# Performance work log

Hardware: AMD Instinct MI355X
Metric: run time of the kernel (lower is better)

The kernel has to match this reference:

```python
import jax, jax.numpy as jnp
import numpy as np

B, T, F = 16, 512, 512
H, D = 8, 64  # heads, key_dim (latent_dim)
EPS = 1e-3    # keras LayerNormalization default epsilon


def layer_norm(x, g, b):
    mu = jnp.mean(x, axis=-1, keepdims=True)
    var = jnp.mean(jnp.square(x - mu), axis=-1, keepdims=True)
    return (x - mu) * jax.lax.rsqrt(var + EPS) * g + b


def setup_inputs() -> dict:
    key = jax.random.key(0)
    ks = jax.random.split(key, 16)
    s = 0.02
    return {
        "x": jax.random.normal(ks[0], (B, T, F), jnp.float32),
        # MultiHeadAttention params (keras layout)
        "Wq": jax.random.normal(ks[1], (F, H, D), jnp.float32) * s,
        "bq": jnp.zeros((H, D), jnp.float32),
        "Wk": jax.random.normal(ks[2], (F, H, D), jnp.float32) * s,
        "bk": jnp.zeros((H, D), jnp.float32),
        "Wv": jax.random.normal(ks[3], (F, H, D), jnp.float32) * s,
        "bv": jnp.zeros((H, D), jnp.float32),
        "Wo": jax.random.normal(ks[4], (H, D, F), jnp.float32) * s,
        "bo": jnp.zeros((F,), jnp.float32),
        "ln1_g": jnp.ones((F,), jnp.float32),
        "ln1_b": jnp.zeros((F,), jnp.float32),
        # GRU (reset_after=True, recurrent_activation=sigmoid, activation=relu)
        "gru_k": jax.random.normal(ks[5], (F, 3 * F), jnp.float32) * s,
        "gru_rk": jax.random.normal(ks[6], (F, 3 * F), jnp.float32) * s,
        "gru_b": jnp.zeros((2, 3 * F), jnp.float32),  # [input_bias, recurrent_bias]
        # Dense
        "Wd": jax.random.normal(ks[7], (F, F), jnp.float32) * s,
        "bd": jnp.zeros((F,), jnp.float32),
        "ln2_g": jnp.ones((F,), jnp.float32),
        "ln2_b": jnp.zeros((F,), jnp.float32),
    }


def mha(x, Wq, bq, Wk, bk, Wv, bv, Wo, bo):
    q = jnp.einsum("btf,fhd->bthd", x, Wq) + bq
    k = jnp.einsum("bsf,fhd->bshd", x, Wk) + bk
    v = jnp.einsum("bsf,fhd->bshd", x, Wv) + bv
    scores = jnp.einsum("bthd,bshd->bhts", q, k) / jnp.sqrt(jnp.float32(D))
    attn = jax.nn.softmax(scores, axis=-1)
    ctx = jnp.einsum("bhts,bshd->bthd", attn, v)
    return jnp.einsum("bthd,hdf->btf", ctx, Wo) + bo


def gru(x, gru_k, gru_rk, gru_b):
    # keras GRU, reset_after=True: precompute input projections once
    xp = x @ gru_k + gru_b[0]            # [B,T,3F]
    rb = gru_b[1]                        # recurrent bias [3F]
    xp_t = jnp.transpose(xp, (1, 0, 2))  # time-major [T,B,3F]

    def step(h, xt):
        rec = h @ gru_rk + rb
        xz, xr, xh = jnp.split(xt, 3, axis=-1)
        rz, rr, rh = jnp.split(rec, 3, axis=-1)
        z = jax.nn.sigmoid(xz + rz)
        r = jax.nn.sigmoid(xr + rr)
        hh = jax.nn.relu(xh + r * rh)    # activation='relu'
        h_new = z * h + (1.0 - z) * hh
        return h_new, h_new

    h0 = jnp.zeros((x.shape[0], gru_rk.shape[0]), x.dtype)
    _, ys = jax.lax.scan(step, h0, xp_t)
    return jnp.transpose(ys, (1, 0, 2))  # [B,T,F]


def reference(x, Wq, bq, Wk, bk, Wv, bv, Wo, bo, ln1_g, ln1_b,
              gru_k, gru_rk, gru_b, Wd, bd, ln2_g, ln2_b):
    a = mha(x, Wq, bq, Wk, bk, Wv, bv, Wo, bo)
    x1 = layer_norm(a + x, ln1_g, ln1_b)
    g = gru(x1, gru_k, gru_rk, gru_b)
    d = g @ Wd + bd
    return layer_norm(d + x1, ln2_g, ln2_b)
```

## Files before the change

kernel.cpp:

```cpp
#include <hip/hip_runtime.h>
#include <math.h>

#define GRID_WGS 128

typedef __attribute__((ext_vector_type(8))) short bf16x8;
typedef __attribute__((ext_vector_type(4))) float f32x4;
typedef __attribute__((ext_vector_type(4))) unsigned short us4;

static __device__ __forceinline__ float sigmoidf_(float x) {
    return 1.0f / (1.0f + __expf(-x));
}
static __device__ __forceinline__ unsigned short f2bf(float f) {
    unsigned int u = __float_as_uint(f);
    u += 0x7fffu + ((u >> 16) & 1u);
    return (unsigned short)(u >> 16);
}
static __device__ __forceinline__ float bfbits2f(unsigned int b) {
    return __uint_as_float(b << 16);
}
static __device__ __forceinline__ void gload_lds16(const void* g, void* l) {
    __builtin_amdgcn_global_load_lds(
        (const __attribute__((address_space(1))) unsigned int*)g,
        (__attribute__((address_space(3))) unsigned int*)l, 16, 0, 0);
}

__global__ __launch_bounds__(256)
void prep(const float* __restrict__ x, unsigned short* __restrict__ xb,
          const float* __restrict__ bq, const float* __restrict__ bk,
          const float* __restrict__ bv, float* __restrict__ bqkv,
          const float* __restrict__ Wq, const float* __restrict__ Wk,
          const float* __restrict__ Wv, const float* __restrict__ Wo,
          const float* __restrict__ gruk, const float* __restrict__ Wd,
          unsigned short* __restrict__ wqkvT, unsigned short* __restrict__ woT,
          unsigned short* __restrict__ gkT, unsigned short* __restrict__ wdT,
          unsigned int* __restrict__ hbufz, unsigned int* __restrict__ Z)
{
    __shared__ float tile[32][33];
    const int bid = blockIdx.x, tid = threadIdx.x;
    if (bid < 4096) {
        const int i = (bid * 256 + tid) * 4;
        const float4 v = *(const float4*)(x + i);
        const us4 o = {f2bf(v.x), f2bf(v.y), f2bf(v.z), f2bf(v.w)};
        *(us4*)(xb + i) = o;
    } else if (bid < 4102) {
        const int i = (bid - 4096) * 256 + tid;
        bqkv[i] = (i < 512) ? bq[i] : ((i < 1024) ? bk[i - 512] : bv[i - 1024]);
    } else if (bid < 6150) {
        int t = bid - 4102;
        const float* in; unsigned short* out; int N;
        if      (t < 256)  { in = Wq;   out = wqkvT;               N = 512;  }
        else if (t < 512)  { in = Wk;   out = wqkvT + 256 * 1024;  N = 512;  t -= 256;  }
        else if (t < 768)  { in = Wv;   out = wqkvT + 512 * 1024;  N = 512;  t -= 512;  }
        else if (t < 1024) { in = Wo;   out = woT;                 N = 512;  t -= 768;  }
        else if (t < 1792) { in = gruk; out = gkT;                 N = 1536; t -= 1024; }
        else               { in = Wd;   out = wdT;                 N = 512;  t -= 1792; }
        const int tilesx = N / 32;
        const int n0 = (t % tilesx) * 32, k0 = (t / tilesx) * 32;
        const int c = tid & 31, r8 = tid >> 5;
#pragma unroll
        for (int i = 0; i < 4; ++i) {
            const int k = r8 + i * 8;
            tile[k][c] = in[(size_t)(k0 + k) * N + n0 + c];
        }
        __syncthreads();
#pragma unroll
        for (int i = 0; i < 4; ++i) {
            const int n = r8 + i * 8;
            out[(size_t)(n0 + n) * 512 + k0 + c] = f2bf(tile[c][n]);
        }
    } else if (bid == 6150) {
        for (int i = tid; i < 8192; i += 256) hbufz[i] = 0u;
    } else {
        for (int i = tid; i < 2048; i += 256) Z[i] = 0u;
    }
}

__global__ __launch_bounds__(256)
void gemm_bf16(const unsigned short* __restrict__ A, const unsigned short* __restrict__ Bt,
               const float* __restrict__ bias, const float* __restrict__ resid,
               float* __restrict__ C, unsigned short* __restrict__ Cb,
               int M, int N, int K)
{
    __shared__ unsigned short As[128 * 64];
    __shared__ unsigned short Bs[128 * 64];
    const int tid = threadIdx.x;
    const int wave = tid >> 6, lane = tid & 63;
    const int bm = blockIdx.x * 128, bn = blockIdx.y * 128;
    const int wr = wave >> 1, wc = wave & 1;
    const int stR = lane >> 3;
    const int stC = (lane & 7) * 8;

    const unsigned short* Abase = A + (size_t)(bm + wave * 32 + stR) * K + stC;
    const unsigned short* Bbase = Bt + (size_t)(bn + wave * 32 + stR) * K + stC;
    unsigned short* AsW = As + wave * 2048;
    unsigned short* BsW = Bs + wave * 2048;

    f32x4 acc[4][4] = {};
    const int fr = lane & 15;
    const int fko = (lane >> 4) * 8;

    for (int k0 = 0; k0 < K; k0 += 64) {
#pragma unroll
        for (int i = 0; i < 4; ++i) {
            gload_lds16(Abase + (size_t)i * 8 * K + k0, AsW + i * 512);
            gload_lds16(Bbase + (size_t)i * 8 * K + k0, BsW + i * 512);
        }
        __syncthreads();
        bf16x8 af[4][2], bfr[4][2];
#pragma unroll
        for (int m = 0; m < 4; ++m) {
            const unsigned short* ap = As + (wr * 64 + m * 16 + fr) * 64 + fko;
            af[m][0] = *(const bf16x8*)(ap);
            af[m][1] = *(const bf16x8*)(ap + 32);
        }
#pragma unroll
        for (int n = 0; n < 4; ++n) {
            const unsigned short* bp = Bs + (wc * 64 + n * 16 + fr) * 64 + fko;
            bfr[n][0] = *(const bf16x8*)(bp);
            bfr[n][1] = *(const bf16x8*)(bp + 32);
        }
#pragma unroll
        for (int m = 0; m < 4; ++m)
#pragma unroll
            for (int n = 0; n < 4; ++n) {
                acc[m][n] = __builtin_amdgcn_mfma_f32_16x16x32_bf16(af[m][0], bfr[n][0], acc[m][n], 0, 0, 0);
                acc[m][n] = __builtin_amdgcn_mfma_f32_16x16x32_bf16(af[m][1], bfr[n][1], acc[m][n], 0, 0, 0);
            }
        __syncthreads();
    }
    const int fq = lane >> 4;
#pragma unroll
    for (int n = 0; n < 4; ++n) {
        const int col = bn + wc * 64 + n * 16 + fr;
        const float bv = bias ? bias[col] : 0.f;
#pragma unroll
        for (int m = 0; m < 4; ++m) {
#pragma unroll
            for (int j = 0; j < 4; ++j) {
                const int row = bm + wr * 64 + m * 16 + fq * 4 + j;
                float v = acc[m][n][j] + bv;
                if (resid) v += resid[(size_t)row * N + col];
                if (C)  C[(size_t)row * N + col] = v;
                if (Cb) Cb[(size_t)row * N + col] = f2bf(v);
            }
        }
    }
}

__global__ __launch_bounds__(256)
void attn_bf16(const unsigned short* __restrict__ qkv, unsigned short* __restrict__ ctxb)
{
    __shared__ unsigned short S[32][512];
    __shared__ float KV[64][69];
    const int tid = threadIdx.x;
    const int wg = blockIdx.x;
    const int qt = wg & 15, h = (wg >> 4) & 7, b = wg >> 7;
    const int r = tid >> 3, oct = tid & 7;
    const int t0 = qt * 32;
    const int ss = tid >> 2, d4 = (tid & 3) * 16;

    float4 qreg[16];
    {
        const unsigned short* qrow = qkv + ((size_t)(b * 512 + t0 + r) * 1536) + h * 64;
#pragma unroll
        for (int i = 0; i < 8; ++i) {
            const bf16x8 v = *(const bf16x8*)(qrow + i * 8);
            qreg[2 * i] = {bfbits2f((unsigned short)v[0]) * 0.125f,
                           bfbits2f((unsigned short)v[1]) * 0.125f,
                           bfbits2f((unsigned short)v[2]) * 0.125f,
                           bfbits2f((unsigned short)v[3]) * 0.125f};
            qreg[2 * i + 1] = {bfbits2f((unsigned short)v[4]) * 0.125f,
                               bfbits2f((unsigned short)v[5]) * 0.125f,
                               bfbits2f((unsigned short)v[6]) * 0.125f,
                               bfbits2f((unsigned short)v[7]) * 0.125f};
        }
    }
    for (int st = 0; st < 8; ++st) {
        {
            const unsigned short* krow =
                qkv + ((size_t)(b * 512 + st * 64 + ss) * 1536) + 512 + h * 64 + d4;
            const bf16x8 v0 = *(const bf16x8*)(krow);
            const bf16x8 v1 = *(const bf16x8*)(krow + 8);
#pragma unroll
            for (int e = 0; e < 8; ++e) {
                KV[ss][d4 + e] = bfbits2f((unsigned short)v0[e]);
                KV[ss][d4 + 8 + e] = bfbits2f((unsigned short)v1[e]);
            }
        }
        __syncthreads();
        float accd[8] = {};
#pragma unroll 4
        for (int kk = 0; kk < 16; ++kk) {
            const float4 qv = qreg[kk];
#pragma unroll
            for (int i = 0; i < 8; ++i) {
                const float4 kv = *(const float4*)&KV[oct * 8 + i][kk * 4];
                accd[i] += qv.x * kv.x + qv.y * kv.y + qv.z * kv.z + qv.w * kv.w;
            }
        }
#pragma unroll
        for (int i = 0; i < 8; ++i)
            S[r][st * 64 + oct * 8 + i] = f2bf(accd[i]);
        __syncthreads();
    }
    const int c0 = oct * 64;
    float mx = -1e30f;
#pragma unroll
    for (int c8 = 0; c8 < 8; ++c8) {
        const bf16x8 sv = *(const bf16x8*)&S[r][c0 + c8 * 8];
#pragma unroll
        for (int e = 0; e < 8; ++e) mx = fmaxf(mx, bfbits2f((unsigned short)sv[e]));
    }
    mx = fmaxf(mx, __shfl_xor(mx, 1));
    mx = fmaxf(mx, __shfl_xor(mx, 2));
    mx = fmaxf(mx, __shfl_xor(mx, 4));
    float sum = 0.f;
#pragma unroll
    for (int c8 = 0; c8 < 8; ++c8) {
        const bf16x8 sv = *(const bf16x8*)&S[r][c0 + c8 * 8];
        us4 o1, o2;
#pragma unroll
        for (int e = 0; e < 8; ++e) {
            const float p = __expf(bfbits2f((unsigned short)sv[e]) - mx);
            sum += p;
            if (e < 4) o1[e] = f2bf(p); else o2[e - 4] = f2bf(p);
        }
        *(us4*)&S[r][c0 + c8 * 8] = o1;
        *(us4*)&S[r][c0 + c8 * 8 + 4] = o2;
    }
    sum += __shfl_xor(sum, 1);
    sum += __shfl_xor(sum, 2);
    sum += __shfl_xor(sum, 4);
    const float inv = 1.0f / sum;
    __syncthreads();
    float o[8] = {};
    for (int st = 0; st < 8; ++st) {
        {
            const unsigned short* vrow =
                qkv + ((size_t)(b * 512 + st * 64 + ss) * 1536) + 1024 + h * 64 + d4;
            const bf16x8 v0 = *(const bf16x8*)(vrow);
            const bf16x8 v1 = *(const bf16x8*)(vrow + 8);
#pragma unroll
            for (int e = 0; e < 8; ++e) {
                KV[ss][d4 + e] = bfbits2f((unsigned short)v0[e]);
                KV[ss][d4 + 8 + e] = bfbits2f((unsigned short)v1[e]);
            }
        }
        __syncthreads();
#pragma unroll 2
        for (int s8 = 0; s8 < 8; ++s8) {
            const bf16x8 pv = *(const bf16x8*)&S[r][st * 64 + s8 * 8];
#pragma unroll
            for (int e = 0; e < 8; ++e) {
                const float p = bfbits2f((unsigned short)pv[e]);
                const float4 k0 = *(const float4*)&KV[s8 * 8 + e][oct * 8];
                const float4 k1 = *(const float4*)&KV[s8 * 8 + e][oct * 8 + 4];
                o[0] = fmaf(p, k0.x, o[0]); o[1] = fmaf(p, k0.y, o[1]);
                o[2] = fmaf(p, k0.z, o[2]); o[3] = fmaf(p, k0.w, o[3]);
                o[4] = fmaf(p, k1.x, o[4]); o[5] = fmaf(p, k1.y, o[5]);
                o[6] = fmaf(p, k1.z, o[6]); o[7] = fmaf(p, k1.w, o[7]);
            }
        }
        __syncthreads();
    }
    unsigned short* crow = ctxb + ((size_t)(b * 512 + t0 + r) * 512) + h * 64 + oct * 8;
    const us4 t1 = {f2bf(o[0] * inv), f2bf(o[1] * inv), f2bf(o[2] * inv), f2bf(o[3] * inv)};
    const us4 t2 = {f2bf(o[4] * inv), f2bf(o[5] * inv), f2bf(o[6] * inv), f2bf(o[7] * inv)};
    *(us4*)(crow) = t1;
    *(us4*)(crow + 4) = t2;
}

__global__ __launch_bounds__(256)
void ln_f32(const float* __restrict__ in, float* __restrict__ out,
            const float* __restrict__ g, const float* __restrict__ bb,
            unsigned short* __restrict__ outb)
{
    const int lane = threadIdx.x & 63;
    const int row = blockIdx.x * 4 + (threadIdx.x >> 6);
    const float* x = in + (size_t)row * 512;
    const float4 a = *(const float4*)(x + lane * 4);
    const float4 c = *(const float4*)(x + 256 + lane * 4);
    float s = a.x + a.y + a.z + a.w + c.x + c.y + c.z + c.w;
#pragma unroll
    for (int off = 1; off < 64; off <<= 1) s += __shfl_xor(s, off);
    const float mu = s * (1.0f / 512.0f);
    float vs = 0.f;
    vs += (a.x - mu) * (a.x - mu) + (a.y - mu) * (a.y - mu);
    vs += (a.z - mu) * (a.z - mu) + (a.w - mu) * (a.w - mu);
    vs += (c.x - mu) * (c.x - mu) + (c.y - mu) * (c.y - mu);
    vs += (c.z - mu) * (c.z - mu) + (c.w - mu) * (c.w - mu);
#pragma unroll
    for (int off = 1; off < 64; off <<= 1) vs += __shfl_xor(vs, off);
    const float rstd = rsqrtf(vs * (1.0f / 512.0f) + 1e-3f);
    const float4 g1 = *(const float4*)(g + lane * 4);
    const float4 g2 = *(const float4*)(g + 256 + lane * 4);
    const float4 b1 = *(const float4*)(bb + lane * 4);
    const float4 b2 = *(const float4*)(bb + 256 + lane * 4);
    float* y = out + (size_t)row * 512;
    const float4 o1 = {(a.x - mu) * rstd * g1.x + b1.x, (a.y - mu) * rstd * g1.y + b1.y,
                       (a.z - mu) * rstd * g1.z + b1.z, (a.w - mu) * rstd * g1.w + b1.w};
    const float4 o2 = {(c.x - mu) * rstd * g2.x + b2.x, (c.y - mu) * rstd * g2.y + b2.y,
                       (c.z - mu) * rstd * g2.z + b2.z, (c.w - mu) * rstd * g2.w + b2.w};
    *(float4*)(y + lane * 4) = o1;
    *(float4*)(y + 256 + lane * 4) = o2;
    if (outb) {
        unsigned short* yb = outb + (size_t)row * 512;
        const us4 p1 = {f2bf(o1.x), f2bf(o1.y), f2bf(o1.z), f2bf(o1.w)};
        const us4 p2 = {f2bf(o2.x), f2bf(o2.y), f2bf(o2.z), f2bf(o2.w)};
        *(us4*)(yb + lane * 4) = p1;
        *(us4*)(yb + 256 + lane * 4) = p2;
    }
}

__global__ __launch_bounds__(256, 1)
void gru_persist(const float* __restrict__ rk,
                 const unsigned short* __restrict__ xpb,
                 const float* __restrict__ rb,
                 unsigned short* __restrict__ hbuf,
                 unsigned short* __restrict__ goutb,
                 unsigned int* __restrict__ bar,
                 unsigned int* __restrict__ ctl)
{
    __shared__ int sh_part, sh_memb;
    const int tid = threadIdx.x;

    if (tid == 0) {
        unsigned int xcc;
        asm("s_getreg_b32 %0, hwreg(HW_REG_XCC_ID)" : "=s"(xcc));
        xcc &= 7u;
        const unsigned int rank =
            __hip_atomic_fetch_add(&ctl[xcc], 1u, __ATOMIC_RELAXED, __HIP_MEMORY_SCOPE_AGENT);
        __hip_atomic_fetch_add(&ctl[8], 1u, __ATOMIC_ACQ_REL, __HIP_MEMORY_SCOPE_AGENT);
        unsigned int spins = 0;
        while (__hip_atomic_load(&ctl[8], __ATOMIC_ACQUIRE, __HIP_MEMORY_SCOPE_AGENT)
               < (unsigned)GRID_WGS) {
            __builtin_amdgcn_s_sleep(1);
            if (++spins > (1u << 20)) break;
        }
        unsigned int cnt[8];
#pragma unroll
        for (int i = 0; i < 8; ++i)
            cnt[i] = __hip_atomic_load(&ctl[i], __ATOMIC_ACQUIRE, __HIP_MEMORY_SCOPE_AGENT);
        int best = 0;
#pragma unroll
        for (int i = 1; i < 8; ++i)
            if (cnt[i] > cnt[best]) best = i;
        sh_part = (xcc == (unsigned)best && rank < 8u) ? 1 : 0;
        sh_memb = (int)rank;
    }
    __syncthreads();
    if (!sh_part) return;
    const int member = sh_memb;

    const int wv = tid >> 6, l = tid & 63;
    const int wgi = member * 4 + wv;
    const int lo16 = l & 15;
    const int hi4 = l >> 4;
    const int gc = wgi * 16 + lo16;

    bf16x8 B[3][16];
#pragma unroll
    for (int g = 0; g < 3; ++g)
#pragma unroll
        for (int kt = 0; kt < 16; ++kt) {
            bf16x8 bv;
#pragma unroll
            for (int j = 0; j < 8; ++j) {
                const int k = kt * 32 + hi4 * 8 + j;
                bv[j] = (short)f2bf(rk[(size_t)k * 1536 + g * 512 + gc]);
            }
            B[g][kt] = bv;
        }
    const float rbz = rb[gc], rbr = rb[512 + gc], rbh = rb[1024 + gc];
    float hst[4] = {0.f, 0.f, 0.f, 0.f};

    float xz[4], xr[4], xh[4];
#pragma unroll
    for (int j = 0; j < 4; ++j) {
        const unsigned short* xrow = xpb + ((size_t)((hi4 * 4 + j) * 512)) * 1536 + gc;
        xz[j] = bfbits2f(xrow[0]); xr[j] = bfbits2f(xrow[512]); xh[j] = bfbits2f(xrow[1024]);
    }
    unsigned int hnb[4] = {0u, 0u, 0u, 0u};

    const unsigned short* ab0 = hbuf + lo16 * 512 + hi4 * 8;
    const unsigned short* ab1 = ab0 + 16 * 512;

    for (int t = 0; t < 512; ++t) {
        const unsigned short* abase = (t & 1) ? ab1 : ab0;
        unsigned short* hw = hbuf + (size_t)((t + 1) & 1) * (16 * 512);
        bf16x8 A[16];
        asm volatile(
            "global_load_dwordx4 %0,  %16, off sc0\n\t"
            "global_load_dwordx4 %1,  %16, off offset:64 sc0\n\t"
            "global_load_dwordx4 %2,  %16, off offset:128 sc0\n\t"
            "global_load_dwordx4 %3,  %16, off offset:192 sc0\n\t"
            "global_load_dwordx4 %4,  %16, off offset:256 sc0\n\t"
            "global_load_dwordx4 %5,  %16, off offset:320 sc0\n\t"
            "global_load_dwordx4 %6,  %16, off offset:384 sc0\n\t"
            "global_load_dwordx4 %7,  %16, off offset:448 sc0\n\t"
            "global_load_dwordx4 %8,  %16, off offset:512 sc0\n\t"
            "global_load_dwordx4 %9,  %16, off offset:576 sc0\n\t"
            "global_load_dwordx4 %10, %16, off offset:640 sc0\n\t"
            "global_load_dwordx4 %11, %16, off offset:704 sc0\n\t"
            "global_load_dwordx4 %12, %16, off offset:768 sc0\n\t"
            "global_load_dwordx4 %13, %16, off offset:832 sc0\n\t"
            "global_load_dwordx4 %14, %16, off offset:896 sc0\n\t"
            "global_load_dwordx4 %15, %16, off offset:960 sc0"
            : "=&v"(A[0]), "=&v"(A[1]), "=&v"(A[2]), "=&v"(A[3]),
              "=&v"(A[4]), "=&v"(A[5]), "=&v"(A[6]), "=&v"(A[7]),
              "=&v"(A[8]), "=&v"(A[9]), "=&v"(A[10]), "=&v"(A[11]),
              "=&v"(A[12]), "=&v"(A[13]), "=&v"(A[14]), "=&v"(A[15])
            : "v"(abase) : "memory");
        unsigned int xnz[4], xnr[4], xnh[4];
        {
            const unsigned short* x0 = xpb + ((size_t)((hi4 * 4 + 0) * 512 + t + 1)) * 1536 + gc;
            const unsigned short* x1 = xpb + ((size_t)((hi4 * 4 + 1) * 512 + t + 1)) * 1536 + gc;
            const unsigned short* x2 = xpb + ((size_t)((hi4 * 4 + 2) * 512 + t + 1)) * 1536 + gc;
            const unsigned short* x3 = xpb + ((size_t)((hi4 * 4 + 3) * 512 + t + 1)) * 1536 + gc;
            asm volatile(
                "global_load_ushort %0,  %12, off\n\t"
                "global_load_ushort %1,  %12, off offset:1024\n\t"
                "global_load_ushort %2,  %12, off offset:2048\n\t"
                "global_load_ushort %3,  %13, off\n\t"
                "global_load_ushort %4,  %13, off offset:1024\n\t"
                "global_load_ushort %5,  %13, off offset:2048\n\t"
                "global_load_ushort %6,  %14, off\n\t"
                "global_load_ushort %7,  %14, off offset:1024\n\t"
                "global_load_ushort %8,  %14, off offset:2048\n\t"
                "global_load_ushort %9,  %15, off\n\t"
                "global_load_ushort %10, %15, off offset:1024\n\t"
                "global_load_ushort %11, %15, off offset:2048"
                : "=&v"(xnz[0]), "=&v"(xnr[0]), "=&v"(xnh[0]),
                  "=&v"(xnz[1]), "=&v"(xnr[1]), "=&v"(xnh[1]),
                  "=&v"(xnz[2]), "=&v"(xnr[2]), "=&v"(xnh[2]),
                  "=&v"(xnz[3]), "=&v"(xnr[3]), "=&v"(xnh[3])
                : "v"(x0), "v"(x1), "v"(x2), "v"(x3) : "memory");
        }
        {
            const int grow = t ? t - 1 : 0;
            unsigned short* g0 = goutb + ((size_t)((hi4 * 4 + 0) * 512 + grow)) * 512 + gc;
            unsigned short* g1 = goutb + ((size_t)((hi4 * 4 + 1) * 512 + grow)) * 512 + gc;
            unsigned short* g2 = goutb + ((size_t)((hi4 * 4 + 2) * 512 + grow)) * 512 + gc;
            unsigned short* g3 = goutb + ((size_t)((hi4 * 4 + 3) * 512 + grow)) * 512 + gc;
            asm volatile(
                "global_store_short %0, %4, off\n\t"
                "global_store_short %1, %5, off\n\t"
                "global_store_short %2, %6, off\n\t"
                "global_store_short %3, %7, off"
                :: "v"(g0), "v"(g1), "v"(g2), "v"(g3),
                   "v"(hnb[0]), "v"(hnb[1]), "v"(hnb[2]), "v"(hnb[3]) : "memory");
        }
        asm volatile("s_waitcnt vmcnt(16)" ::: "memory");
        __builtin_amdgcn_sched_barrier(0);

        f32x4 accz = {0.f, 0.f, 0.f, 0.f};
        f32x4 accr = {0.f, 0.f, 0.f, 0.f};
        f32x4 acch = {0.f, 0.f, 0.f, 0.f};
#pragma unroll
        for (int kt = 0; kt < 16; ++kt) {
            accz = __builtin_amdgcn_mfma_f32_16x16x32_bf16(A[kt], B[0][kt], accz, 0, 0, 0);
            accr = __builtin_amdgcn_mfma_f32_16x16x32_bf16(A[kt], B[1][kt], accr, 0, 0, 0);
            acch = __builtin_amdgcn_mfma_f32_16x16x32_bf16(A[kt], B[2][kt], acch, 0, 0, 0);
        }
#pragma unroll
        for (int j = 0; j < 4; ++j) {
            const int b = hi4 * 4 + j;
            const float z = sigmoidf_(xz[j] + accz[j] + rbz);
            const float r = sigmoidf_(xr[j] + accr[j] + rbr);
            const float hh = fmaxf(xh[j] + r * (acch[j] + rbh), 0.f);
            const float hnew = z * hst[j] + (1.f - z) * hh;
            hst[j] = hnew;
            const unsigned short hb = f2bf(hnew);
            hnb[j] = (unsigned int)hb;
            hw[b * 512 + gc] = hb;
        }
        asm volatile("s_waitcnt vmcnt(0)" ::: "memory");
        __builtin_amdgcn_sched_barrier(0);
#pragma unroll
        for (int j = 0; j < 4; ++j) {
            xz[j] = bfbits2f(xnz[j]); xr[j] = bfbits2f(xnr[j]); xh[j] = bfbits2f(xnh[j]);
        }
        if (t < 511) {
            __syncthreads();
            if (tid == 0) {
                __hip_atomic_fetch_add(bar, 1u, __ATOMIC_RELAXED, __HIP_MEMORY_SCOPE_AGENT);
                const unsigned int target = 8u * (unsigned int)(t + 1);
                unsigned int it = 0;
                while (__hip_atomic_load(bar, __ATOMIC_RELAXED, __HIP_MEMORY_SCOPE_AGENT)
                       < target) {
                    if (++it > (1u << 14)) break;
                }
                if (it > (1u << 14)) {
                    unsigned int cur = 0, it2 = 0;
                    do {
                        asm volatile("global_atomic_add %0, %1, %2, off sc0\n\t"
                                     "s_waitcnt vmcnt(0)"
                                     : "=v"(cur) : "v"(bar), "v"(0u) : "memory");
                        if (++it2 > (1u << 15)) break;
                    } while (cur < target);
                }
            }
            __syncthreads();
        }
    }
#pragma unroll
    for (int j = 0; j < 4; ++j)
        goutb[((size_t)((hi4 * 4 + j) * 512 + 511)) * 512 + gc] = (unsigned short)hnb[j];
}

extern "C" void kernel_launch(void* const* d_in, const int* in_sizes, int n_in,
                              void* d_out, int out_size, void* d_ws, size_t ws_size,
                              hipStream_t stream)
{
    const float* x     = (const float*)d_in[0];
    const float* Wq    = (const float*)d_in[1];
    const float* bq    = (const float*)d_in[2];
    const float* Wk    = (const float*)d_in[3];
    const float* bk    = (const float*)d_in[4];
    const float* Wv    = (const float*)d_in[5];
    const float* bv    = (const float*)d_in[6];
    const float* Wo    = (const float*)d_in[7];
    const float* bo    = (const float*)d_in[8];
    const float* ln1g  = (const float*)d_in[9];
    const float* ln1b  = (const float*)d_in[10];
    const float* gruk  = (const float*)d_in[11];
    const float* grurk = (const float*)d_in[12];
    const float* grub  = (const float*)d_in[13];
    const float* Wd    = (const float*)d_in[14];
    const float* bd    = (const float*)d_in[15];
    const float* ln2g  = (const float*)d_in[16];
    const float* ln2b  = (const float*)d_in[17];
    float* out = (float*)d_out;

    char* base = (char*)d_ws;
    const size_t MB = 1024 * 1024;
    unsigned short* qkvb = (unsigned short*)base;
    unsigned short* xpb  = (unsigned short*)base;
    float*          dout = (float*)(base + 24 * MB);
    float*          R4   = (float*)(base + 48 * MB);
    unsigned short* S1   = (unsigned short*)(base + 64 * MB);
    unsigned short* WT   = (unsigned short*)(base + 72 * MB);
    unsigned short* wqkvT = WT;
    unsigned short* woT  = WT + 768 * 1024;
    unsigned short* gkT  = WT + 1024 * 1024;
    unsigned short* wdT  = WT + 1792 * 1024;
    unsigned short* hbuf = (unsigned short*)(base + 76 * MB);
    char*           Z    = base + 76 * MB + 64 * 1024;
    unsigned int*   ctl  = (unsigned int*)(Z);
    unsigned int*   bar  = (unsigned int*)(Z + 256);
    float*          bqkv = (float*)(base + 77 * MB);

    const dim3 blk(256);
    const dim3 g512(8192 / 128, 512 / 128);
    const dim3 g1536(8192 / 128, 1536 / 128);

    prep<<<dim3(6152), blk, 0, stream>>>(x, S1, bq, bk, bv, bqkv,
                                         Wq, Wk, Wv, Wo, gruk, Wd,
                                         wqkvT, woT, gkT, wdT,
                                         (unsigned int*)hbuf, (unsigned int*)Z);
    gemm_bf16<<<g1536, blk, 0, stream>>>(S1, wqkvT, bqkv, nullptr, nullptr, qkvb, 8192, 1536, 512);
    attn_bf16<<<dim3(2048), blk, 0, stream>>>(qkvb, S1);
    gemm_bf16<<<g512, blk, 0, stream>>>(S1, woT, bo, x, R4, nullptr, 8192, 512, 512);
    ln_f32<<<dim3(2048), blk, 0, stream>>>(R4, R4, ln1g, ln1b, S1);
    gemm_bf16<<<g1536, blk, 0, stream>>>(S1, gkT, grub, nullptr, nullptr, xpb, 8192, 1536, 512);
    gru_persist<<<dim3(GRID_WGS), blk, 0, stream>>>(grurk, xpb, grub + 1536, hbuf, S1, bar, ctl);
    gemm_bf16<<<g512, blk, 0, stream>>>(S1, wdT, bd, R4, dout, nullptr, 8192, 512, 512);
    ln_f32<<<dim3(2048), blk, 0, stream>>>(dout, out, ln2g, ln2b, nullptr);
}
```

Baseline: 2.317 ms.

## Rewrite attention kernel with bf16 MFMA for QK^T and PV

```diff
diff --git a/kernel.cpp b/kernel.cpp
--- a/kernel.cpp
+++ b/kernel.cpp
@@ -147,127 +147,121 @@
     }
 }
 
-__global__ __launch_bounds__(256)
-void attn_bf16(const unsigned short* __restrict__ qkv, unsigned short* __restrict__ ctxb)
+__global__ __launch_bounds__(128)
+void attn_mfma(const unsigned short* __restrict__ qkv, unsigned short* __restrict__ ctxb)
 {
-    __shared__ unsigned short S[32][512];
-    __shared__ float KV[64][69];
+    __shared__ unsigned short P[32][520];
+    __shared__ unsigned short KV[64][72];
+    __shared__ float invs[32];
     const int tid = threadIdx.x;
     const int wg = blockIdx.x;
     const int qt = wg & 15, h = (wg >> 4) & 7, b = wg >> 7;
-    const int r = tid >> 3, oct = tid & 7;
     const int t0 = qt * 32;
-    const int ss = tid >> 2, d4 = (tid & 3) * 16;
-
-    float4 qreg[16];
+    const int w = tid >> 6, lane = tid & 63;
+    const int lo16 = lane & 15, hi4 = lane >> 4;
+
+    bf16x8 Aq0, Aq1;
     {
-        const unsigned short* qrow = qkv + ((size_t)(b * 512 + t0 + r) * 1536) + h * 64;
-#pragma unroll
-        for (int i = 0; i < 8; ++i) {
-            const bf16x8 v = *(const bf16x8*)(qrow + i * 8);
-            qreg[2 * i] = {bfbits2f((unsigned short)v[0]) * 0.125f,
-                           bfbits2f((unsigned short)v[1]) * 0.125f,
-                           bfbits2f((unsigned short)v[2]) * 0.125f,
-                           bfbits2f((unsigned short)v[3]) * 0.125f};
-            qreg[2 * i + 1] = {bfbits2f((unsigned short)v[4]) * 0.125f,
-                               bfbits2f((unsigned short)v[5]) * 0.125f,
-                               bfbits2f((unsigned short)v[6]) * 0.125f,
-                               bfbits2f((unsigned short)v[7]) * 0.125f};
-        }
-    }
+        const unsigned short* qrow =
+            qkv + ((size_t)(b * 512 + t0 + w * 16 + lo16)) * 1536 + h * 64 + hi4 * 8;
+        Aq0 = *(const bf16x8*)(qrow);
+        Aq1 = *(const bf16x8*)(qrow + 32);
+    }
+    const int ss = tid >> 1, sh = tid & 1;
+
     for (int st = 0; st < 8; ++st) {
         {
             const unsigned short* krow =
-                qkv + ((size_t)(b * 512 + st * 64 + ss) * 1536) + 512 + h * 64 + d4;
-            const bf16x8 v0 = *(const bf16x8*)(krow);
-            const bf16x8 v1 = *(const bf16x8*)(krow + 8);
+                qkv + ((size_t)(b * 512 + st * 64 + ss)) * 1536 + 512 + h * 64 + sh * 32;
+            *(bf16x8*)&KV[ss][sh * 32]      = *(const bf16x8*)(krow);
+            *(bf16x8*)&KV[ss][sh * 32 + 8]  = *(const bf16x8*)(krow + 8);
+            *(bf16x8*)&KV[ss][sh * 32 + 16] = *(const bf16x8*)(krow + 16);
+            *(bf16x8*)&KV[ss][sh * 32 + 24] = *(const bf16x8*)(krow + 24);
+        }
+        __syncthreads();
+#pragma unroll
+        for (int n = 0; n < 4; ++n) {
+            const bf16x8 b0 = *(const bf16x8*)&KV[n * 16 + lo16][hi4 * 8];
+            const bf16x8 b1 = *(const bf16x8*)&KV[n * 16 + lo16][32 + hi4 * 8];
+            f32x4 acc = {0.f, 0.f, 0.f, 0.f};
+            acc = __builtin_amdgcn_mfma_f32_16x16x32_bf16(Aq0, b0, acc, 0, 0, 0);
+            acc = __builtin_amdgcn_mfma_f32_16x16x32_bf16(Aq1, b1, acc, 0, 0, 0);
+#pragma unroll
+            for (int j = 0; j < 4; ++j)
+                P[w * 16 + hi4 * 4 + j][st * 64 + n * 16 + lo16] = f2bf(acc[j]);
+        }
+        __syncthreads();
+    }
+    {
+        const int r = tid >> 2, quad = tid & 3;
+        const int c0 = quad * 128;
+        float mx = -1e30f;
+#pragma unroll
+        for (int c8 = 0; c8 < 16; ++c8) {
+            const bf16x8 sv = *(const bf16x8*)&P[r][c0 + c8 * 8];
+#pragma unroll
+            for (int e = 0; e < 8; ++e) mx = fmaxf(mx, bfbits2f((unsigned short)sv[e]));
+        }
+        mx = fmaxf(mx, __shfl_xor(mx, 1));
+        mx = fmaxf(mx, __shfl_xor(mx, 2));
+        mx *= 0.125f;
+        float sum = 0.f;
+#pragma unroll
+        for (int c8 = 0; c8 < 16; ++c8) {
+            const bf16x8 sv = *(const bf16x8*)&P[r][c0 + c8 * 8];
+            us4 o1, o2;
 #pragma unroll
             for (int e = 0; e < 8; ++e) {
-                KV[ss][d4 + e] = bfbits2f((unsigned short)v0[e]);
-                KV[ss][d4 + 8 + e] = bfbits2f((unsigned short)v1[e]);
+                const float p = __expf(bfbits2f((unsigned short)sv[e]) * 0.125f - mx);
+                sum += p;
+                if (e < 4) o1[e] = f2bf(p); else o2[e - 4] = f2bf(p);
             }
-        }
-        __syncthreads();
-        float accd[8] = {};
-#pragma unroll 4
-        for (int kk = 0; kk < 16; ++kk) {
-            const float4 qv = qreg[kk];
-#pragma unroll
-            for (int i = 0; i < 8; ++i) {
-                const float4 kv = *(const float4*)&KV[oct * 8 + i][kk * 4];
-                accd[i] += qv.x * kv.x + qv.y * kv.y + qv.z * kv.z + qv.w * kv.w;
-            }
-        }
-#pragma unroll
-        for (int i = 0; i < 8; ++i)
-            S[r][st * 64 + oct * 8 + i] = f2bf(accd[i]);
-        __syncthreads();
-    }
-    const int c0 = oct * 64;
-    float mx = -1e30f;
-#pragma unroll
-    for (int c8 = 0; c8 < 8; ++c8) {
-        const bf16x8 sv = *(const bf16x8*)&S[r][c0 + c8 * 8];
-#pragma unroll
-        for (int e = 0; e < 8; ++e) mx = fmaxf(mx, bfbits2f((unsigned short)sv[e]));
-    }
-    mx = fmaxf(mx, __shfl_xor(mx, 1));
-    mx = fmaxf(mx, __shfl_xor(mx, 2));
-    mx = fmaxf(mx, __shfl_xor(mx, 4));
-    float sum = 0.f;
-#pragma unroll
-    for (int c8 = 0; c8 < 8; ++c8) {
-        const bf16x8 sv = *(const bf16x8*)&S[r][c0 + c8 * 8];
-        us4 o1, o2;
-#pragma unroll
-        for (int e = 0; e < 8; ++e) {
-            const float p = __expf(bfbits2f((unsigned short)sv[e]) - mx);
-            sum += p;
-            if (e < 4) o1[e] = f2bf(p); else o2[e - 4] = f2bf(p);
-        }
-        *(us4*)&S[r][c0 + c8 * 8] = o1;
-        *(us4*)&S[r][c0 + c8 * 8 + 4] = o2;
-    }
-    sum += __shfl_xor(sum, 1);
-    sum += __shfl_xor(sum, 2);
-    sum += __shfl_xor(sum, 4);
-    const float inv = 1.0f / sum;
+            *(us4*)&P[r][c0 + c8 * 8] = o1;
+            *(us4*)&P[r][c0 + c8 * 8 + 4] = o2;
+        }
+        sum += __shfl_xor(sum, 1);
+        sum += __shfl_xor(sum, 2);
+        if (quad == 0) invs[r] = 1.0f / sum;
+    }
     __syncthreads();
-    float o[8] = {};
+    f32x4 oac[4] = {};
     for (int st = 0; st < 8; ++st) {
         {
             const unsigned short* vrow =
-                qkv + ((size_t)(b * 512 + st * 64 + ss) * 1536) + 1024 + h * 64 + d4;
+                qkv + ((size_t)(b * 512 + st * 64 + ss)) * 1536 + 1024 + h * 64 + sh * 32;
             const bf16x8 v0 = *(const bf16x8*)(vrow);
             const bf16x8 v1 = *(const bf16x8*)(vrow + 8);
+            const bf16x8 v2 = *(const bf16x8*)(vrow + 16);
+            const bf16x8 v3 = *(const bf16x8*)(vrow + 24);
 #pragma unroll
             for (int e = 0; e < 8; ++e) {
-                KV[ss][d4 + e] = bfbits2f((unsigned short)v0[e]);
-                KV[ss][d4 + 8 + e] = bfbits2f((unsigned short)v1[e]);
+                KV[sh * 32 + e][ss]      = (unsigned short)v0[e];
+                KV[sh * 32 + 8 + e][ss]  = (unsigned short)v1[e];
+                KV[sh * 32 + 16 + e][ss] = (unsigned short)v2[e];
+                KV[sh * 32 + 24 + e][ss] = (unsigned short)v3[e];
             }
         }
         __syncthreads();
-#pragma unroll 2
-        for (int s8 = 0; s8 < 8; ++s8) {
-            const bf16x8 pv = *(const bf16x8*)&S[r][st * 64 + s8 * 8];
-#pragma unroll
-            for (int e = 0; e < 8; ++e) {
-                const float p = bfbits2f((unsigned short)pv[e]);
-                const float4 k0 = *(const float4*)&KV[s8 * 8 + e][oct * 8];
-                const float4 k1 = *(const float4*)&KV[s8 * 8 + e][oct * 8 + 4];
-                o[0] = fmaf(p, k0.x, o[0]); o[1] = fmaf(p, k0.y, o[1]);
-                o[2] = fmaf(p, k0.z, o[2]); o[3] = fmaf(p, k0.w, o[3]);
-                o[4] = fmaf(p, k1.x, o[4]); o[5] = fmaf(p, k1.y, o[5]);
-                o[6] = fmaf(p, k1.z, o[6]); o[7] = fmaf(p, k1.w, o[7]);
-            }
-        }
-        __syncthreads();
-    }
-    unsigned short* crow = ctxb + ((size_t)(b * 512 + t0 + r) * 512) + h * 64 + oct * 8;
-    const us4 t1 = {f2bf(o[0] * inv), f2bf(o[1] * inv), f2bf(o[2] * inv), f2bf(o[3] * inv)};
-    const us4 t2 = {f2bf(o[4] * inv), f2bf(o[5] * inv), f2bf(o[6] * inv), f2bf(o[7] * inv)};
-    *(us4*)(crow) = t1;
-    *(us4*)(crow + 4) = t2;
+        const bf16x8 pa0 = *(const bf16x8*)&P[w * 16 + lo16][st * 64 + hi4 * 8];
+        const bf16x8 pa1 = *(const bf16x8*)&P[w * 16 + lo16][st * 64 + 32 + hi4 * 8];
+#pragma unroll
+        for (int n = 0; n < 4; ++n) {
+            const bf16x8 b0 = *(const bf16x8*)&KV[n * 16 + lo16][hi4 * 8];
+            const bf16x8 b1 = *(const bf16x8*)&KV[n * 16 + lo16][32 + hi4 * 8];
+            oac[n] = __builtin_amdgcn_mfma_f32_16x16x32_bf16(pa0, b0, oac[n], 0, 0, 0);
+            oac[n] = __builtin_amdgcn_mfma_f32_16x16x32_bf16(pa1, b1, oac[n], 0, 0, 0);
+        }
+        __syncthreads();
+    }
+#pragma unroll
+    for (int n = 0; n < 4; ++n) {
+#pragma unroll
+        for (int j = 0; j < 4; ++j) {
+            const int q = w * 16 + hi4 * 4 + j;
+            ctxb[((size_t)(b * 512 + t0 + q)) * 512 + h * 64 + n * 16 + lo16] =
+                f2bf(oac[n][j] * invs[q]);
+        }
+    }
 }
 
 __global__ __launch_bounds__(256)
@@ -559,7 +553,7 @@
                                          wqkvT, woT, gkT, wdT,
                                          (unsigned int*)hbuf, (unsigned int*)Z);
     gemm_bf16<<<g1536, blk, 0, stream>>>(S1, wqkvT, bqkv, nullptr, nullptr, qkvb, 8192, 1536, 512);
-    attn_bf16<<<dim3(2048), blk, 0, stream>>>(qkvb, S1);
+    attn_mfma<<<dim3(2048), dim3(128), 0, stream>>>(qkvb, S1);
     gemm_bf16<<<g512, blk, 0, stream>>>(S1, woT, bo, x, R4, nullptr, 8192, 512, 512);
     ln_f32<<<dim3(2048), blk, 0, stream>>>(R4, R4, ln1g, ln1b, S1);
     gemm_bf16<<<g1536, blk, 0, stream>>>(S1, gkT, grub, nullptr, nullptr, xpb, 8192, 1536, 512);
```

After: 1.911 ms, median of 2. 17.5% less time.
